# Performance work log

Measured on AMD Instinct MI355X. Metric: run time of the kernel, lower is better.

Reference implementation:

```python
import jax, jax.numpy as jnp
import numpy as np

N_NODES = 50000
N_EDGES = 800000
D = 128
NEG_SLOPE = 0.01
LN_EPS = 1e-5


def gcn_conv(x, W, b, src, dst, n_nodes):
    # Linear transform: [N, D_in] @ [D_in, D_out]
    h = x @ W
    # Symmetric degree normalization (self-loops already included in src/dst)
    deg = jax.ops.segment_sum(jnp.ones_like(dst, dtype=h.dtype), dst, num_segments=n_nodes)
    dinv = jnp.where(deg > 0, jax.lax.rsqrt(deg), 0.0)
    coef = dinv[src] * dinv[dst]                      # [E]
    msg = h[src] * coef[:, None]                      # gather + scale, [E, D]
    out = jax.ops.segment_sum(msg, dst, num_segments=n_nodes)  # scatter-add
    return out + b


def layer_norm(x, gamma, beta):
    mu = jnp.mean(x, axis=-1, keepdims=True)
    var = jnp.mean(jnp.square(x - mu), axis=-1, keepdims=True)
    return (x - mu) * jax.lax.rsqrt(var + LN_EPS) * gamma + beta


def setup_inputs() -> dict:
    key = jax.random.key(0)
    ks = jax.random.split(key, 8)
    x = jax.random.normal(ks[0], (N_NODES, D), dtype=jnp.float32)
    edge_index = jax.random.randint(ks[1], (2, N_EDGES), 0, N_NODES, dtype=jnp.int64)
    s = 1.0 / np.sqrt(D)
    W1 = jax.random.uniform(ks[2], (D, D), jnp.float32, -s, s)
    b1 = jnp.zeros((D,), jnp.float32)
    W2 = jax.random.uniform(ks[3], (D, D), jnp.float32, -s, s)
    b2 = jnp.zeros((D,), jnp.float32)
    ln1_g = jnp.ones((D,), jnp.float32)
    ln1_b = jnp.zeros((D,), jnp.float32)
    ln2_g = jnp.ones((D,), jnp.float32)
    ln2_b = jnp.zeros((D,), jnp.float32)
    return {"x": x, "edge_index": edge_index, "W1": W1, "b1": b1,
            "ln1_g": ln1_g, "ln1_b": ln1_b, "W2": W2, "b2": b2,
            "ln2_g": ln2_g, "ln2_b": ln2_b}


def reference(x, edge_index, W1, b1, ln1_g, ln1_b, W2, b2, ln2_g, ln2_b):
    n = x.shape[0]
    # add self-loops (PyG GCNConv default)
    loops = jnp.arange(n, dtype=edge_index.dtype)
    src = jnp.concatenate([edge_index[0], loops])
    dst = jnp.concatenate([edge_index[1], loops])

    residual = x
    h = gcn_conv(x, W1, b1, src, dst, n)
    h = jax.nn.leaky_relu(h, NEG_SLOPE)
    h = layer_norm(h + residual, ln1_g, ln1_b)
    h = gcn_conv(h, W2, b2, src, dst, n)
    return jax.nn.leaky_relu(layer_norm(h + residual, ln2_g, ln2_b), NEG_SLOPE)
```

## Files before the change

kernel.cpp:

```cpp
#include <hip/hip_runtime.h>
#include <hip/hip_bf16.h>

#define NN 50000
#define NE 800000
#define D 128
#define NEG_SLOPE 0.01f
#define LN_EPS 1e-5f

#define NPB 256
#define NB 196
#define CAP 6144
#define ECH 6144
#define NCH ((NE + ECH - 1) / ECH)
#define NDEG 256
#define NGEMM ((NN + 63) / 64)

typedef __attribute__((ext_vector_type(8))) short bf16x8;
typedef __attribute__((ext_vector_type(4))) float f32x4;
typedef __attribute__((ext_vector_type(4))) int i32x4;

__device__ inline unsigned short f2bf(float f) {
    unsigned u = __float_as_uint(f);
    unsigned r = 0x7FFFu + ((u >> 16) & 1u);
    return (unsigned short)((u + r) >> 16);
}
__device__ inline void bf2x(unsigned u, float& lo, float& hi) {
    lo = __uint_as_float(u << 16);
    hi = __uint_as_float(u & 0xFFFF0000u);
}


struct BucketLDS {
    int2 stage[ECH];
    int hist[NB], lofs[NB], lcur[NB], gbase[NB];
    int tmp[256];
};
struct GemmLDS {
    unsigned short a[64 * 128];
    unsigned short w[128 * 128];
};
union FusedLDS { BucketLDS b; GemmLDS g; };

__device__ inline void gemm_body(GemmLDS& L, const float* __restrict__ A,
                                 const unsigned short* __restrict__ WT,
                                 unsigned short* __restrict__ out, int m0, int n, int t) {
    #pragma unroll
    for (int it = 0; it < 8; ++it) {
        int idx = it * 256 + t;
        int row = idx >> 4, c = idx & 15;
        uint4 v = *(const uint4*)&WT[row * 128 + c * 8];
        int byte = (row * 256 + c * 16) ^ ((row & 7) << 4);
        *(uint4*)((char*)L.w + byte) = v;
    }
    #pragma unroll
    for (int it = 0; it < 4; ++it) {
        int idx = it * 256 + t;
        int row = idx >> 4, c = idx & 15;
        int grow = m0 + row;
        uint4 w = make_uint4(0u, 0u, 0u, 0u);
        if (grow < n) {
            float4 v0 = *(const float4*)&A[(size_t)grow * D + c * 8];
            float4 v1 = *(const float4*)&A[(size_t)grow * D + c * 8 + 4];
            w.x = (unsigned)f2bf(v0.x) | ((unsigned)f2bf(v0.y) << 16);
            w.y = (unsigned)f2bf(v0.z) | ((unsigned)f2bf(v0.w) << 16);
            w.z = (unsigned)f2bf(v1.x) | ((unsigned)f2bf(v1.y) << 16);
            w.w = (unsigned)f2bf(v1.z) | ((unsigned)f2bf(v1.w) << 16);
        }
        int byte = (row * 256 + c * 16) ^ ((row & 7) << 4);
        *(uint4*)((char*)L.a + byte) = w;
    }
    __syncthreads();

    int wv = t >> 6, l = t & 63;
    int lrow = l & 15, lgrp = l >> 4;
    int arow = wv * 16 + lrow;

    f32x4 acc[8];
    #pragma unroll
    for (int nf = 0; nf < 8; ++nf) acc[nf] = (f32x4){0.f, 0.f, 0.f, 0.f};

    #pragma unroll
    for (int kk = 0; kk < 4; ++kk) {
        int abyte = (arow * 256 + kk * 64 + lgrp * 16) ^ ((arow & 7) << 4);
        bf16x8 afrag = *(bf16x8*)((char*)L.a + abyte);
        #pragma unroll
        for (int nf = 0; nf < 8; ++nf) {
            int bcol = nf * 16 + lrow;
            int bbyte = (bcol * 256 + kk * 64 + lgrp * 16) ^ ((bcol & 7) << 4);
            bf16x8 bfrag = *(bf16x8*)((char*)L.w + bbyte);
            acc[nf] = __builtin_amdgcn_mfma_f32_16x16x32_bf16(afrag, bfrag, acc[nf], 0, 0, 0);
        }
    }

    #pragma unroll
    for (int nf = 0; nf < 8; ++nf) {
        #pragma unroll
        for (int r = 0; r < 4; ++r) {
            int grow = m0 + wv * 16 + lgrp * 4 + r;
            if (grow < n) out[(size_t)grow * D + nf * 16 + lrow] = f2bf(acc[nf][r]);
        }
    }
}

__global__ __launch_bounds__(256) void fused1(const int* __restrict__ src,
                                              const int* __restrict__ dst,
                                              int* __restrict__ bcursor,
                                              int2* __restrict__ bedge,
                                              int* __restrict__ deg,
                                              const float* __restrict__ x,
                                              const unsigned short* __restrict__ wt1,
                                              unsigned short* __restrict__ hbf) {
    __shared__ FusedLDS u;
    int bid = blockIdx.x, t = threadIdx.x;

    if (bid < NCH) {
        BucketLDS& L = u.b;
        int e0 = bid * ECH;
        int ecnt = min(ECH, NE - e0);
        if (t < NB) L.hist[t] = 0;
        __syncthreads();
        for (int k = t; k < ecnt; k += 256) atomicAdd(&L.hist[dst[e0 + k] >> 8], 1);
        __syncthreads();
        int v = (t < NB) ? L.hist[t] : 0;
        L.tmp[t] = v;
        __syncthreads();
        for (int off = 1; off < 256; off <<= 1) {
            int uu = (t >= off) ? L.tmp[t - off] : 0;
            __syncthreads();
            L.tmp[t] += uu;
            __syncthreads();
        }
        if (t < NB) {
            L.lofs[t] = L.tmp[t] - v;
            L.lcur[t] = L.tmp[t] - v;
            L.gbase[t] = atomicAdd(&bcursor[t], v);
        }
        __syncthreads();
        for (int k = t; k < ecnt; k += 256) {
            int s = src[e0 + k], d = dst[e0 + k];
            int p = atomicAdd(&L.lcur[d >> 8], 1);
            L.stage[p] = make_int2(s, d);
        }
        __syncthreads();
        for (int k = t; k < ecnt; k += 256) {
            int2 eg = L.stage[k];
            int b = eg.y >> 8;
            bedge[(size_t)b * CAP + L.gbase[b] + (k - L.lofs[b])] = eg;
        }
    } else if (bid < NCH + NDEG) {
        for (int k = (bid - NCH) * 256 + t; k < NE; k += NDEG * 256)
            atomicAdd(&deg[dst[k]], 1);
    } else {
        gemm_body(u.g, x, wt1, hbf, (bid - NCH - NDEG) * 64, NN, t);
    }
}

__global__ __launch_bounds__(256) void fused2(const int2* __restrict__ bedge,
                                              const int* __restrict__ bcnt,
                                              const int* __restrict__ deg,
                                              float* __restrict__ dinv,
                                              int2* __restrict__ rowinfo,
                                              int* __restrict__ ticket,
                                              int2* __restrict__ csr_pair) {
    __shared__ int tmp[256];
    __shared__ int rl[NPB], cur[NPB];
    __shared__ float sdinv[NPB];
    __shared__ int base;
    int b = blockIdx.x, t = threadIdx.x;
    int node = b * NPB + t;
    int dg = (node < NN) ? deg[node] : 0;
    float dv = rsqrtf((float)(dg + 1));
    sdinv[t] = dv;
    int pdeg = (dg + 7) & ~7;
    tmp[t] = pdeg;
    __syncthreads();
    for (int off = 1; off < 256; off <<= 1) {
        int uu = (t >= off) ? tmp[t - off] : 0;
        __syncthreads();
        tmp[t] += uu;
        __syncthreads();
    }
    if (t == 255) base = atomicAdd(ticket, tmp[255]);
    __syncthreads();
    int start = base + tmp[t] - pdeg;
    rl[t] = start;
    cur[t] = 0;
    if (node < NN) {
        dinv[node] = dv;
        rowinfo[node] = make_int2(start, pdeg);
    }
    __syncthreads();
    int s0 = b * CAP, s1 = s0 + bcnt[b];
    for (int k = s0 + t; k < s1; k += 256) {
        int2 eg = bedge[k];
        int li = eg.y & 255;
        int p = atomicAdd(&cur[li], 1);
        int ds = deg[eg.x];
        float coef = rsqrtf((float)(ds + 1)) * sdinv[li];
        csr_pair[rl[li] + p] = make_int2(eg.x, __float_as_int(coef));
    }
    __syncthreads();
    int dgc = cur[t];
    int pend = (dgc + 7) & ~7;
    int selfsrc = (node < NN) ? node : 0;
    for (int k = dgc; k < pend; ++k)
        csr_pair[rl[t] + k] = make_int2(selfsrc, 0);
}

__global__ void wt_pack2(const float* __restrict__ W1, const float* __restrict__ W2,
                         unsigned short* __restrict__ WT1, unsigned short* __restrict__ WT2) {
    int tid = blockIdx.x * 256 + threadIdx.x;
    const float* W = (tid < D * D) ? W1 : W2;
    unsigned short* WT = (tid < D * D) ? WT1 : WT2;
    int id = tid & (D * D - 1);
    int nn = id & 127, k = id >> 7;
    WT[nn * 128 + k] = f2bf(W[k * 128 + nn]);
}


__device__ inline void agg8(const unsigned* __restrict__ h, const int2* __restrict__ csr_pair,
                            int e, int lane, float& accx, float& accy) {
    i32x4 q0 = __builtin_nontemporal_load((const i32x4*)(csr_pair + e + 0));
    i32x4 q1 = __builtin_nontemporal_load((const i32x4*)(csr_pair + e + 2));
    i32x4 q2 = __builtin_nontemporal_load((const i32x4*)(csr_pair + e + 4));
    i32x4 q3 = __builtin_nontemporal_load((const i32x4*)(csr_pair + e + 6));
    unsigned g0 = h[(size_t)q0[0] * (D / 2) + lane];
    unsigned g1 = h[(size_t)q0[2] * (D / 2) + lane];
    unsigned g2 = h[(size_t)q1[0] * (D / 2) + lane];
    unsigned g3 = h[(size_t)q1[2] * (D / 2) + lane];
    unsigned g4 = h[(size_t)q2[0] * (D / 2) + lane];
    unsigned g5 = h[(size_t)q2[2] * (D / 2) + lane];
    unsigned g6 = h[(size_t)q3[0] * (D / 2) + lane];
    unsigned g7 = h[(size_t)q3[2] * (D / 2) + lane];
    float ax, ay, c;
    c = __int_as_float(q0[1]); bf2x(g0, ax, ay); accx = fmaf(c, ax, accx); accy = fmaf(c, ay, accy);
    c = __int_as_float(q0[3]); bf2x(g1, ax, ay); accx = fmaf(c, ax, accx); accy = fmaf(c, ay, accy);
    c = __int_as_float(q1[1]); bf2x(g2, ax, ay); accx = fmaf(c, ax, accx); accy = fmaf(c, ay, accy);
    c = __int_as_float(q1[3]); bf2x(g3, ax, ay); accx = fmaf(c, ax, accx); accy = fmaf(c, ay, accy);
    c = __int_as_float(q2[1]); bf2x(g4, ax, ay); accx = fmaf(c, ax, accx); accy = fmaf(c, ay, accy);
    c = __int_as_float(q2[3]); bf2x(g5, ax, ay); accx = fmaf(c, ax, accx); accy = fmaf(c, ay, accy);
    c = __int_as_float(q3[1]); bf2x(g6, ax, ay); accx = fmaf(c, ax, accx); accy = fmaf(c, ay, accy);
    c = __int_as_float(q3[3]); bf2x(g7, ax, ay); accx = fmaf(c, ax, accx); accy = fmaf(c, ay, accy);
}

__device__ inline void agg_2node(const unsigned* __restrict__ h,
                                 const int2* __restrict__ csr_pair,
                                 int eA, int eA1, int eB, int eB1, int lane,
                                 float& aAx, float& aAy, float& aBx, float& aBy) {
    while (eA < eA1 && eB < eB1) {
        i32x4 qA0 = __builtin_nontemporal_load((const i32x4*)(csr_pair + eA + 0));
        i32x4 qA1 = __builtin_nontemporal_load((const i32x4*)(csr_pair + eA + 2));
        i32x4 qA2 = __builtin_nontemporal_load((const i32x4*)(csr_pair + eA + 4));
        i32x4 qA3 = __builtin_nontemporal_load((const i32x4*)(csr_pair + eA + 6));
        i32x4 qB0 = __builtin_nontemporal_load((const i32x4*)(csr_pair + eB + 0));
        i32x4 qB1 = __builtin_nontemporal_load((const i32x4*)(csr_pair + eB + 2));
        i32x4 qB2 = __builtin_nontemporal_load((const i32x4*)(csr_pair + eB + 4));
        i32x4 qB3 = __builtin_nontemporal_load((const i32x4*)(csr_pair + eB + 6));
        unsigned gA0 = h[(size_t)qA0[0] * (D / 2) + lane];
        unsigned gA1 = h[(size_t)qA0[2] * (D / 2) + lane];
        unsigned gA2 = h[(size_t)qA1[0] * (D / 2) + lane];
        unsigned gA3 = h[(size_t)qA1[2] * (D / 2) + lane];
        unsigned gA4 = h[(size_t)qA2[0] * (D / 2) + lane];
        unsigned gA5 = h[(size_t)qA2[2] * (D / 2) + lane];
        unsigned gA6 = h[(size_t)qA3[0] * (D / 2) + lane];
        unsigned gA7 = h[(size_t)qA3[2] * (D / 2) + lane];
        unsigned gB0 = h[(size_t)qB0[0] * (D / 2) + lane];
        unsigned gB1 = h[(size_t)qB0[2] * (D / 2) + lane];
        unsigned gB2 = h[(size_t)qB1[0] * (D / 2) + lane];
        unsigned gB3 = h[(size_t)qB1[2] * (D / 2) + lane];
        unsigned gB4 = h[(size_t)qB2[0] * (D / 2) + lane];
        unsigned gB5 = h[(size_t)qB2[2] * (D / 2) + lane];
        unsigned gB6 = h[(size_t)qB3[0] * (D / 2) + lane];
        unsigned gB7 = h[(size_t)qB3[2] * (D / 2) + lane];
        float ax, ay, c;
        c = __int_as_float(qA0[1]); bf2x(gA0, ax, ay); aAx = fmaf(c, ax, aAx); aAy = fmaf(c, ay, aAy);
        c = __int_as_float(qA0[3]); bf2x(gA1, ax, ay); aAx = fmaf(c, ax, aAx); aAy = fmaf(c, ay, aAy);
        c = __int_as_float(qA1[1]); bf2x(gA2, ax, ay); aAx = fmaf(c, ax, aAx); aAy = fmaf(c, ay, aAy);
        c = __int_as_float(qA1[3]); bf2x(gA3, ax, ay); aAx = fmaf(c, ax, aAx); aAy = fmaf(c, ay, aAy);
        c = __int_as_float(qA2[1]); bf2x(gA4, ax, ay); aAx = fmaf(c, ax, aAx); aAy = fmaf(c, ay, aAy);
        c = __int_as_float(qA2[3]); bf2x(gA5, ax, ay); aAx = fmaf(c, ax, aAx); aAy = fmaf(c, ay, aAy);
        c = __int_as_float(qA3[1]); bf2x(gA6, ax, ay); aAx = fmaf(c, ax, aAx); aAy = fmaf(c, ay, aAy);
        c = __int_as_float(qA3[3]); bf2x(gA7, ax, ay); aAx = fmaf(c, ax, aAx); aAy = fmaf(c, ay, aAy);
        c = __int_as_float(qB0[1]); bf2x(gB0, ax, ay); aBx = fmaf(c, ax, aBx); aBy = fmaf(c, ay, aBy);
        c = __int_as_float(qB0[3]); bf2x(gB1, ax, ay); aBx = fmaf(c, ax, aBx); aBy = fmaf(c, ay, aBy);
        c = __int_as_float(qB1[1]); bf2x(gB2, ax, ay); aBx = fmaf(c, ax, aBx); aBy = fmaf(c, ay, aBy);
        c = __int_as_float(qB1[3]); bf2x(gB3, ax, ay); aBx = fmaf(c, ax, aBx); aBy = fmaf(c, ay, aBy);
        c = __int_as_float(qB2[1]); bf2x(gB4, ax, ay); aBx = fmaf(c, ax, aBx); aBy = fmaf(c, ay, aBy);
        c = __int_as_float(qB2[3]); bf2x(gB5, ax, ay); aBx = fmaf(c, ax, aBx); aBy = fmaf(c, ay, aBy);
        c = __int_as_float(qB3[1]); bf2x(gB6, ax, ay); aBx = fmaf(c, ax, aBx); aBy = fmaf(c, ay, aBy);
        c = __int_as_float(qB3[3]); bf2x(gB7, ax, ay); aBx = fmaf(c, ax, aBx); aBy = fmaf(c, ay, aBy);
        eA += 8; eB += 8;
    }
    while (eA < eA1) { agg8(h, csr_pair, eA, lane, aAx, aAy); eA += 8; }
    while (eB < eB1) { agg8(h, csr_pair, eB, lane, aBx, aBy); eB += 8; }
}

__global__ __launch_bounds__(512) void agg_ln1_gemm(const unsigned* __restrict__ h,
                                                    const float* __restrict__ x,
                                                    const float* __restrict__ bias,
                                                    const float* __restrict__ gamma,
                                                    const float* __restrict__ beta,
                                                    const float* __restrict__ dinv,
                                                    const int2* __restrict__ rowinfo,
                                                    const int2* __restrict__ csr_pair,
                                                    const unsigned short* __restrict__ wt2,
                                                    unsigned short* __restrict__ hbf2) {
    __shared__ __align__(16) unsigned short w_lds[128 * 128];
    __shared__ __align__(16) unsigned short a_lds[16 * 128];
    int t = threadIdx.x;

    #pragma unroll
    for (int it = 0; it < 4; ++it) {
        int idx = it * 512 + t;
        int row = idx >> 4, c = idx & 15;
        uint4 v = *(const uint4*)&wt2[row * 128 + c * 8];
        int byte = (row * 256 + c * 16) ^ ((row & 7) << 4);
        *(uint4*)((char*)w_lds + byte) = v;
    }

    int wid = t >> 6, lane = t & 63;
    int iA = blockIdx.x * 16 + wid * 2;
    int iB = iA + 1;
    float diA = dinv[iA], diB = dinv[iB];

    float hx, hy;
    bf2x(h[(size_t)iA * (D / 2) + lane], hx, hy);
    float aAx = diA * diA * hx, aAy = diA * diA * hy;
    bf2x(h[(size_t)iB * (D / 2) + lane], hx, hy);
    float aBx = diB * diB * hx, aBy = diB * diB * hy;

    int2 riA = rowinfo[iA];
    int2 riB = rowinfo[iB];
    int eA = __builtin_amdgcn_readfirstlane(riA.x);
    int eA1 = eA + __builtin_amdgcn_readfirstlane(riA.y);
    int eB = __builtin_amdgcn_readfirstlane(riB.x);
    int eB1 = eB + __builtin_amdgcn_readfirstlane(riB.y);
    agg_2node(h, csr_pair, eA, eA1, eB, eB1, lane, aAx, aAy, aBx, aBy);

    float2 bv = *(const float2*)&bias[2 * lane];
    float2 gv = *(const float2*)&gamma[2 * lane];
    float2 bt = *(const float2*)&beta[2 * lane];

    aAx += bv.x; aAy += bv.y;
    aBx += bv.x; aBy += bv.y;
    aAx = aAx > 0.f ? aAx : NEG_SLOPE * aAx;
    aAy = aAy > 0.f ? aAy : NEG_SLOPE * aAy;
    aBx = aBx > 0.f ? aBx : NEG_SLOPE * aBx;
    aBy = aBy > 0.f ? aBy : NEG_SLOPE * aBy;

    size_t rowA = (size_t)iA * D + 2 * lane;
    size_t rowB = (size_t)iB * D + 2 * lane;
    float2 xA = *(const float2*)&x[rowA];
    float2 xB = *(const float2*)&x[rowB];
    float vA0 = aAx + xA.x, vA1 = aAy + xA.y;
    float vB0 = aBx + xB.x, vB1 = aBy + xB.y;

    float sA1 = vA0 + vA1, sA2 = vA0 * vA0 + vA1 * vA1;
    float sB1 = vB0 + vB1, sB2 = vB0 * vB0 + vB1 * vB1;
    #pragma unroll
    for (int off = 1; off < 64; off <<= 1) {
        sA1 += __shfl_xor(sA1, off, 64);
        sA2 += __shfl_xor(sA2, off, 64);
        sB1 += __shfl_xor(sB1, off, 64);
        sB2 += __shfl_xor(sB2, off, 64);
    }
    float muA = sA1 * (1.f / 128.f);
    float varA = fmaxf(sA2 * (1.f / 128.f) - muA * muA, 0.f);
    float rsA = rsqrtf(varA + LN_EPS);
    float muB = sB1 * (1.f / 128.f);
    float varB = fmaxf(sB2 * (1.f / 128.f) - muB * muB, 0.f);
    float rsB = rsqrtf(varB + LN_EPS);

    float oA0 = (vA0 - muA) * rsA * gv.x + bt.x;
    float oA1 = (vA1 - muA) * rsA * gv.y + bt.y;
    float oB0 = (vB0 - muB) * rsB * gv.x + bt.x;
    float oB1 = (vB1 - muB) * rsB * gv.y + bt.y;

    int rA = wid * 2, rB = wid * 2 + 1;
    unsigned dwA = (unsigned)f2bf(oA0) | ((unsigned)f2bf(oA1) << 16);
    unsigned dwB = (unsigned)f2bf(oB0) | ((unsigned)f2bf(oB1) << 16);
    int byteA = (rA * 256 + lane * 4) ^ ((rA & 7) << 4);
    int byteB = (rB * 256 + lane * 4) ^ ((rB & 7) << 4);
    *(unsigned*)((char*)a_lds + byteA) = dwA;
    *(unsigned*)((char*)a_lds + byteB) = dwB;
    __syncthreads();

    int lrow = lane & 15, lgrp = lane >> 4;
    f32x4 acc = (f32x4){0.f, 0.f, 0.f, 0.f};
    #pragma unroll
    for (int kk = 0; kk < 4; ++kk) {
        int abyte = (lrow * 256 + kk * 64 + lgrp * 16) ^ ((lrow & 7) << 4);
        bf16x8 afrag = *(bf16x8*)((char*)a_lds + abyte);
        int bcol = wid * 16 + lrow;
        int bbyte = (bcol * 256 + kk * 64 + lgrp * 16) ^ ((bcol & 7) << 4);
        bf16x8 bfrag = *(bf16x8*)((char*)w_lds + bbyte);
        acc = __builtin_amdgcn_mfma_f32_16x16x32_bf16(afrag, bfrag, acc, 0, 0, 0);
    }
    #pragma unroll
    for (int r = 0; r < 4; ++r) {
        int grow = blockIdx.x * 16 + lgrp * 4 + r;
        hbf2[(size_t)grow * D + wid * 16 + lrow] = f2bf(acc[r]);
    }
}

__global__ __launch_bounds__(256) void agg_ln2(const unsigned* __restrict__ h,
                                               const float* __restrict__ x,
                                               const float* __restrict__ bias,
                                               const float* __restrict__ gamma,
                                               const float* __restrict__ beta,
                                               const float* __restrict__ dinv,
                                               const int2* __restrict__ rowinfo,
                                               const int2* __restrict__ csr_pair,
                                               float* __restrict__ out) {
    int wid = threadIdx.x >> 6;
    int lane = threadIdx.x & 63;
    int iA = blockIdx.x * 8 + wid * 2;
    int iB = iA + 1;
    float diA = dinv[iA], diB = dinv[iB];

    float hx, hy;
    bf2x(h[(size_t)iA * (D / 2) + lane], hx, hy);
    float aAx = diA * diA * hx, aAy = diA * diA * hy;
    bf2x(h[(size_t)iB * (D / 2) + lane], hx, hy);
    float aBx = diB * diB * hx, aBy = diB * diB * hy;

    int2 riA = rowinfo[iA];
    int2 riB = rowinfo[iB];
    int eA = __builtin_amdgcn_readfirstlane(riA.x);
    int eA1 = eA + __builtin_amdgcn_readfirstlane(riA.y);
    int eB = __builtin_amdgcn_readfirstlane(riB.x);
    int eB1 = eB + __builtin_amdgcn_readfirstlane(riB.y);
    agg_2node(h, csr_pair, eA, eA1, eB, eB1, lane, aAx, aAy, aBx, aBy);

    float2 bv = *(const float2*)&bias[2 * lane];
    float2 gv = *(const float2*)&gamma[2 * lane];
    float2 bt = *(const float2*)&beta[2 * lane];

    aAx += bv.x; aAy += bv.y;
    aBx += bv.x; aBy += bv.y;
    size_t rowA = (size_t)iA * D + 2 * lane;
    size_t rowB = (size_t)iB * D + 2 * lane;
    float2 xA = *(const float2*)&x[rowA];
    float2 xB = *(const float2*)&x[rowB];
    float vA0 = aAx + xA.x, vA1 = aAy + xA.y;
    float vB0 = aBx + xB.x, vB1 = aBy + xB.y;

    float sA1 = vA0 + vA1, sA2 = vA0 * vA0 + vA1 * vA1;
    float sB1 = vB0 + vB1, sB2 = vB0 * vB0 + vB1 * vB1;
    #pragma unroll
    for (int off = 1; off < 64; off <<= 1) {
        sA1 += __shfl_xor(sA1, off, 64);
        sA2 += __shfl_xor(sA2, off, 64);
        sB1 += __shfl_xor(sB1, off, 64);
        sB2 += __shfl_xor(sB2, off, 64);
    }
    float muA = sA1 * (1.f / 128.f);
    float varA = fmaxf(sA2 * (1.f / 128.f) - muA * muA, 0.f);
    float rsA = rsqrtf(varA + LN_EPS);
    float muB = sB1 * (1.f / 128.f);
    float varB = fmaxf(sB2 * (1.f / 128.f) - muB * muB, 0.f);
    float rsB = rsqrtf(varB + LN_EPS);

    float oA0 = (vA0 - muA) * rsA * gv.x + bt.x;
    float oA1 = (vA1 - muA) * rsA * gv.y + bt.y;
    float oB0 = (vB0 - muB) * rsB * gv.x + bt.x;
    float oB1 = (vB1 - muB) * rsB * gv.y + bt.y;
    oA0 = oA0 > 0.f ? oA0 : NEG_SLOPE * oA0;
    oA1 = oA1 > 0.f ? oA1 : NEG_SLOPE * oA1;
    oB0 = oB0 > 0.f ? oB0 : NEG_SLOPE * oB0;
    oB1 = oB1 > 0.f ? oB1 : NEG_SLOPE * oB1;
    *(float2*)&out[rowA] = make_float2(oA0, oA1);
    *(float2*)&out[rowB] = make_float2(oB0, oB1);
}

extern "C" void kernel_launch(void* const* d_in, const int* in_sizes, int n_in,
                              void* d_out, int out_size, void* d_ws, size_t ws_size,
                              hipStream_t stream) {
    const float* x    = (const float*)d_in[0];
    const int*   ei   = (const int*)d_in[1];
    const float* W1   = (const float*)d_in[2];
    const float* b1   = (const float*)d_in[3];
    const float* ln1g = (const float*)d_in[4];
    const float* ln1b = (const float*)d_in[5];
    const float* W2   = (const float*)d_in[6];
    const float* b2   = (const float*)d_in[7];
    const float* ln2g = (const float*)d_in[8];
    const float* ln2b = (const float*)d_in[9];
    float* out = (float*)d_out;

    const int* srcp = ei;
    const int* dstp = ei + NE;

    char* ws = (char*)d_ws;
    size_t p = 0;
    auto alloc = [&](size_t bytes) {
        char* r = ws + p;
        p += (bytes + 255) & ~(size_t)255;
        return r;
    };
    int*   deg      = (int*)alloc(NN * 4);
    int*   bcursor  = (int*)alloc((NB + 1) * 4);
    int2*  rowinfo  = (int2*)alloc((size_t)NN * 8);
    float* dinv     = (float*)alloc(NN * 4);
    int2*  bedge    = (int2*)alloc((size_t)NB * CAP * 8);
    int2*  csr_pair = (int2*)alloc(((size_t)NE + 8 * NN) * 8);
    unsigned short* hbf  = (unsigned short*)alloc((size_t)NN * D * 2);
    unsigned short* hbf2 = (unsigned short*)alloc((size_t)NN * D * 2);
    unsigned short* wt1  = (unsigned short*)alloc(D * D * 2);
    unsigned short* wt2  = (unsigned short*)alloc(D * D * 2);

    size_t zbytes = (char*)rowinfo - (char*)deg;
    hipMemsetAsync(deg, 0, zbytes, stream);

    wt_pack2<<<2 * D * D / 256, 256, 0, stream>>>(W1, W2, wt1, wt2);

    fused1<<<NCH + NDEG + NGEMM, 256, 0, stream>>>(srcp, dstp, bcursor, bedge, deg,
                                                   x, wt1, hbf);

    fused2<<<NB, 256, 0, stream>>>(bedge, bcursor, deg, dinv, rowinfo,
                                   &bcursor[NB], csr_pair);

    agg_ln1_gemm<<<NN / 16, 512, 0, stream>>>((const unsigned*)hbf, x, b1, ln1g, ln1b,
                                              dinv, rowinfo, csr_pair, wt2, hbf2);

    agg_ln2<<<NN / 8, 256, 0, stream>>>((const unsigned*)hbf2, x, b2, ln2g, ln2b,
                                        dinv, rowinfo, csr_pair, out);
}
```

Baseline: 143.4 us.

## Drop LDS staging in edge bucketing and read GEMM weights directly from global

The bucketing phase no longer stages edges in LDS and runs a prefix scan. Each edge now claims a slot with a per-bucket LDS atomic and writes straight to its global bucket, and the edge chunk size grows from 6144 to 8192. The GEMM path stops copying the 128x128 weight matrix into LDS and loads MFMA B fragments directly from global or cache. Together these shrink the union LDS footprint for higher occupancy and remove scan barriers, at the cost of less coalesced scattered global writes and repeated global weight reads per block.

```diff
diff --git a/kernel.cpp b/kernel.cpp
--- a/kernel.cpp
+++ b/kernel.cpp
@@ -10,7 +10,7 @@
 #define NPB 256
 #define NB 196
 #define CAP 6144
-#define ECH 6144
+#define ECH 8192
 #define NCH ((NE + ECH - 1) / ECH)
 #define NDEG 256
 #define NGEMM ((NN + 63) / 64)
@@ -31,27 +31,17 @@
 
 
 struct BucketLDS {
-    int2 stage[ECH];
-    int hist[NB], lofs[NB], lcur[NB], gbase[NB];
+    int hist[NB], lcur[NB], gbase[NB];
     int tmp[256];
 };
 struct GemmLDS {
     unsigned short a[64 * 128];
-    unsigned short w[128 * 128];
 };
 union FusedLDS { BucketLDS b; GemmLDS g; };
 
 __device__ inline void gemm_body(GemmLDS& L, const float* __restrict__ A,
                                  const unsigned short* __restrict__ WT,
                                  unsigned short* __restrict__ out, int m0, int n, int t) {
-    #pragma unroll
-    for (int it = 0; it < 8; ++it) {
-        int idx = it * 256 + t;
-        int row = idx >> 4, c = idx & 15;
-        uint4 v = *(const uint4*)&WT[row * 128 + c * 8];
-        int byte = (row * 256 + c * 16) ^ ((row & 7) << 4);
-        *(uint4*)((char*)L.w + byte) = v;
-    }
     #pragma unroll
     for (int it = 0; it < 4; ++it) {
         int idx = it * 256 + t;
@@ -86,8 +76,7 @@
         #pragma unroll
         for (int nf = 0; nf < 8; ++nf) {
             int bcol = nf * 16 + lrow;
-            int bbyte = (bcol * 256 + kk * 64 + lgrp * 16) ^ ((bcol & 7) << 4);
-            bf16x8 bfrag = *(bf16x8*)((char*)L.w + bbyte);
+            bf16x8 bfrag = *(const bf16x8*)&WT[bcol * 128 + kk * 32 + lgrp * 8];
             acc[nf] = __builtin_amdgcn_mfma_f32_16x16x32_bf16(afrag, bfrag, acc[nf], 0, 0, 0);
         }
     }
@@ -121,31 +110,16 @@
         __syncthreads();
         for (int k = t; k < ecnt; k += 256) atomicAdd(&L.hist[dst[e0 + k] >> 8], 1);
         __syncthreads();
-        int v = (t < NB) ? L.hist[t] : 0;
-        L.tmp[t] = v;
-        __syncthreads();
-        for (int off = 1; off < 256; off <<= 1) {
-            int uu = (t >= off) ? L.tmp[t - off] : 0;
-            __syncthreads();
-            L.tmp[t] += uu;
-            __syncthreads();
-        }
         if (t < NB) {
-            L.lofs[t] = L.tmp[t] - v;
-            L.lcur[t] = L.tmp[t] - v;
-            L.gbase[t] = atomicAdd(&bcursor[t], v);
+            L.gbase[t] = atomicAdd(&bcursor[t], L.hist[t]);
+            L.lcur[t] = 0;
         }
         __syncthreads();
         for (int k = t; k < ecnt; k += 256) {
             int s = src[e0 + k], d = dst[e0 + k];
-            int p = atomicAdd(&L.lcur[d >> 8], 1);
-            L.stage[p] = make_int2(s, d);
-        }
-        __syncthreads();
-        for (int k = t; k < ecnt; k += 256) {
-            int2 eg = L.stage[k];
-            int b = eg.y >> 8;
-            bedge[(size_t)b * CAP + L.gbase[b] + (k - L.lofs[b])] = eg;
+            int b = d >> 8;
+            int p = atomicAdd(&L.lcur[b], 1);
+            bedge[(size_t)b * CAP + L.gbase[b] + p] = make_int2(s, d);
         }
     } else if (bid < NCH + NDEG) {
         for (int k = (bid - NCH) * 256 + t; k < NE; k += NDEG * 256)
```

New measurement: 149.8 us. 4.5% more time.
